# Optimization experiments

Hardware: AMD Instinct MI355X
Metric: run time of the kernel (lower is better)

The kernel has to match this reference:

```python
import jax, jax.numpy as jnp
import numpy as np

B, S, D, H = 4, 2048, 1024, 16
HD = D // H
EPS = 1e-5
MASKED_BIAS = -10000.0

def setup_inputs() -> dict:
    key = jax.random.key(0)
    ks = jax.random.split(key, 12)
    sd = 0.02
    return {
        "hidden_states": jax.random.normal(ks[0], (B, S, D), jnp.float32),
        "Wq": jax.random.normal(ks[1], (D, D), jnp.float32) * sd,
        "bq": jnp.zeros((D,), jnp.float32),
        "Wk": jax.random.normal(ks[2], (D, D), jnp.float32) * sd,
        "bk": jnp.zeros((D,), jnp.float32),
        "Wv": jax.random.normal(ks[3], (D, D), jnp.float32) * sd,
        "bv": jnp.zeros((D,), jnp.float32),
        "Wp": jax.random.normal(ks[4], (D, D), jnp.float32) * sd,
        "bp": jnp.zeros((D,), jnp.float32),
        "ln_g": jnp.ones((D,), jnp.float32),
        "ln_b": jnp.zeros((D,), jnp.float32),
    }

def reference(hidden_states, Wq, bq, Wk, bk, Wv, bv, Wp, bp, ln_g, ln_b):
    x = hidden_states  # [B,S,D]
    # QKV projections (nn.Linear: x @ W^T + b; here W stored as [D,D], use x@W)
    q = x @ Wq + bq
    k = x @ Wk + bk
    v = x @ Wv + bv
    # split heads -> [B,H,S,HD]
    def split(t):
        return t.reshape(B, S, H, HD).transpose(0, 2, 1, 3)
    q, k, v = split(q), split(k), split(v)
    # scaled scores [B,H,S,S]
    scores = jnp.einsum("bhqd,bhkd->bhqk", q, k) / jnp.float32(np.sqrt(HD))
    causal = jnp.tril(jnp.ones((S, S), bool))
    scores = jnp.where(causal[None, None], scores, jnp.float32(MASKED_BIAS))
    attn = jax.nn.softmax(scores, axis=-1)
    out = jnp.einsum("bhqk,bhkd->bhqd", attn, v)
    # merge heads -> [B,S,D]
    out = out.transpose(0, 2, 1, 3).reshape(B, S, D)
    out = out @ Wp + bp
    # residual + layernorm
    y = out + x
    mu = jnp.mean(y, axis=-1, keepdims=True)
    var = jnp.var(y, axis=-1, keepdims=True)
    y = (y - mu) * jax.lax.rsqrt(var + EPS) * ln_g + ln_b
    return y
```

## Files before the change

### kernel.cpp

```cpp
#include <hip/hip_runtime.h>
#include <math.h>

#define B_  4
#define S_  2048
#define D_  1024
#define H_  16
#define HD_ 64
#define M_  (B_*S_)

typedef unsigned int  uint;
typedef unsigned short ushort;

typedef __attribute__((ext_vector_type(8))) short bf16x8;
typedef __attribute__((ext_vector_type(4))) float f32x4;

#if __has_builtin(__builtin_amdgcn_exp2f)
#define EXP2(x) __builtin_amdgcn_exp2f(x)
#else
#define EXP2(x) exp2f(x)
#endif

__device__ __forceinline__ ushort f2bf(float x) {
    uint u = __float_as_uint(x);
    u += 0x7FFFu + ((u >> 16) & 1u);
    return (ushort)(u >> 16);
}
__device__ __forceinline__ uint pack2bf(float a, float b) {
    uint ua = __float_as_uint(a); ua += 0x7FFFu + ((ua >> 16) & 1u);
    uint ub = __float_as_uint(b); ub += 0x7FFFu + ((ub >> 16) & 1u);
    return (ua >> 16) | (ub & 0xFFFF0000u);
}

__global__ __launch_bounds__(256) void prep(const float* __restrict__ x,
                                            ushort* __restrict__ xb,
                                            const float* __restrict__ Wq,
                                            const float* __restrict__ Wk,
                                            const float* __restrict__ Wv,
                                            const float* __restrict__ Wp,
                                            ushort* __restrict__ wtq,
                                            ushort* __restrict__ wtk,
                                            ushort* __restrict__ wtv,
                                            ushort* __restrict__ wtp) {
    __shared__ float t[32][33];
    const int tid = threadIdx.x;
    if (blockIdx.z == 0) {
        const int idx = blockIdx.x * 256 + tid;
        const float4* p = (const float4*)(x + (size_t)idx * 8);
        float4 a = p[0], b = p[1];
        uint4 o;
        o.x = pack2bf(a.x, a.y); o.y = pack2bf(a.z, a.w);
        o.z = pack2bf(b.x, b.y); o.w = pack2bf(b.z, b.w);
        ((uint4*)xb)[idx] = o;
    } else {
        const int w = blockIdx.x >> 10;
        const int sub = blockIdx.x & 1023;
        const float* W = (w == 0) ? Wq : (w == 1) ? Wk : (w == 2) ? Wv : Wp;
        ushort* Wt     = (w == 0) ? wtq : (w == 1) ? wtk : (w == 2) ? wtv : wtp;
        const int nb = (sub & 31) * 32, kb = (sub >> 5) * 32;
        #pragma unroll
        for (int l = 0; l < 4; ++l) {
            int idx = tid + l * 256;
            int r = idx >> 5, c = idx & 31;
            t[r][c] = W[(size_t)(kb + r) * D_ + nb + c];
        }
        __syncthreads();
        #pragma unroll
        for (int l = 0; l < 4; ++l) {
            int idx = tid + l * 256;
            int nr = idx >> 5, kc = idx & 31;
            Wt[(size_t)(nb + nr) * D_ + kb + kc] = f2bf(t[kc][nr]);
        }
    }
}

#define GM 128
#define GN 128
#define GK 64

struct GemmLds {
    ushort As[GM * GK];
    ushort Bs[GN * GK];
};

template <bool SWAP>
__device__ __forceinline__ void gemm_core(GemmLds& L,
                                          const ushort* __restrict__ A,
                                          const ushort* __restrict__ Bt,
                                          f32x4 acc[4][4], int m0, int n0) {
    const int tid  = threadIdx.x;
    const int wave = tid >> 6, lane = tid & 63;
    const int wm = (wave >> 1) * 64, wn = (wave & 1) * 64;
    const int fr = lane & 15, fq = lane >> 4;
    const int xrw = (fr & 7) << 4;

    int sg[4];
    #pragma unroll
    for (int it = 0; it < 4; ++it) {
        const int o = (it * 256 + tid) * 16;
        const int r = o >> 7, c = o & 127;
        sg[it] = r * (D_ * 2) + (c ^ ((r & 7) << 4));
    }

    #pragma unroll
    for (int i = 0; i < 4; ++i)
        #pragma unroll
        for (int j = 0; j < 4; ++j) acc[i][j] = (f32x4){0.f, 0.f, 0.f, 0.f};

    const char* Ab = (const char*)A + (size_t)m0 * (D_ * 2);
    const char* Bb = (const char*)Bt + (size_t)n0 * (D_ * 2);

    for (int k0 = 0; k0 < D_; k0 += GK) {
        #pragma unroll
        for (int it = 0; it < 4; ++it) {
            __builtin_amdgcn_global_load_lds(
                (const __attribute__((address_space(1))) void*)(Ab + k0 * 2 + sg[it]),
                (__attribute__((address_space(3))) void*)(&L.As[(it * 256 + wave * 64) * 8]), 16, 0, 0);
            __builtin_amdgcn_global_load_lds(
                (const __attribute__((address_space(1))) void*)(Bb + k0 * 2 + sg[it]),
                (__attribute__((address_space(3))) void*)(&L.Bs[(it * 256 + wave * 64) * 8]), 16, 0, 0);
        }
        __syncthreads();

        #pragma unroll
        for (int kk = 0; kk < 2; ++kk) {
            bf16x8 af[4], bfr[4];
            #pragma unroll
            for (int i = 0; i < 4; ++i)
                af[i] = *(const bf16x8*)((const char*)L.As + (wm + 16 * i + fr) * 128 + ((kk * 64 + fq * 16) ^ xrw));
            #pragma unroll
            for (int j = 0; j < 4; ++j)
                bfr[j] = *(const bf16x8*)((const char*)L.Bs + (wn + 16 * j + fr) * 128 + ((kk * 64 + fq * 16) ^ xrw));
            #pragma unroll
            for (int i = 0; i < 4; ++i)
                #pragma unroll
                for (int j = 0; j < 4; ++j)
                    acc[i][j] = SWAP
                        ? __builtin_amdgcn_mfma_f32_16x16x32_bf16(bfr[j], af[i], acc[i][j], 0, 0, 0)
                        : __builtin_amdgcn_mfma_f32_16x16x32_bf16(af[i], bfr[j], acc[i][j], 0, 0, 0);
        }
        __syncthreads();
    }
}

__global__ __launch_bounds__(256) void gemm_qkvt(const ushort* __restrict__ xb,
                                                 const ushort* __restrict__ wtq,
                                                 const ushort* __restrict__ wtk,
                                                 const ushort* __restrict__ wtv,
                                                 const float* __restrict__ bq,
                                                 const float* __restrict__ bk,
                                                 const float* __restrict__ bv,
                                                 ushort* __restrict__ qb,
                                                 ushort* __restrict__ kb,
                                                 ushort* __restrict__ vtb) {
    __shared__ __align__(16) GemmLds L;
    const int z = blockIdx.z;
    const int lane = threadIdx.x & 63, wave = threadIdx.x >> 6;
    const int wm = (wave >> 1) * 64, wn = (wave & 1) * 64;
    const int cc = lane & 15, fq = lane >> 4;
    const int m0 = blockIdx.x * GM, n0 = blockIdx.y * GN;
    f32x4 acc[4][4];

    if (z < 2) {
        gemm_core<true>(L, xb, z ? wtk : wtq, acc, m0, n0);
        const float* bias = z ? bk : bq;
        ushort* C = z ? kb : qb;
        const float sc = z ? 1.0f : 0.18033688f;
        #pragma unroll
        for (int j = 0; j < 4; ++j) {
            const int f0 = n0 + wn + 16 * j + fq * 4;
            const float4 bs4 = *(const float4*)&bias[f0];
            const int h = f0 >> 6, hd = f0 & 63;
            #pragma unroll
            for (int i = 0; i < 4; ++i) {
                const int token = m0 + wm + 16 * i + cc;
                const int bb = token >> 11, s = token & 2047;
                const float v0 = (acc[i][j][0] + bs4.x) * sc;
                const float v1 = (acc[i][j][1] + bs4.y) * sc;
                const float v2 = (acc[i][j][2] + bs4.z) * sc;
                const float v3 = (acc[i][j][3] + bs4.w) * sc;
                uint2 w; w.x = pack2bf(v0, v1); w.y = pack2bf(v2, v3);
                *(uint2*)&C[(((size_t)bb * H_ + h) * S_ + s) * HD_ + hd] = w;
            }
        }
    } else {
        gemm_core<false>(L, xb, wtv, acc, m0, n0);
        #pragma unroll
        for (int i = 0; i < 4; ++i) {
            const int t0 = m0 + wm + 16 * i + fq * 4;
            const int bb = t0 >> 11, s = t0 & 2047;
            #pragma unroll
            for (int j = 0; j < 4; ++j) {
                const int f = n0 + wn + 16 * j + cc;
                const float bs = bv[f];
                const int h = f >> 6, hd = f & 63;
                uint2 w;
                w.x = pack2bf(acc[i][j][0] + bs, acc[i][j][1] + bs);
                w.y = pack2bf(acc[i][j][2] + bs, acc[i][j][3] + bs);
                *(uint2*)&vtb[(((size_t)bb * H_ + h) * HD_ + hd) * S_ + s] = w;
            }
        }
    }
}

__global__ __launch_bounds__(256) void gemm_p(const ushort* __restrict__ A,
                                              const ushort* __restrict__ Bt,
                                              const float* __restrict__ bias,
                                              float* __restrict__ C) {
    __shared__ __align__(16) GemmLds L;
    const int m0 = blockIdx.y * GM, n0 = blockIdx.x * GN;
    f32x4 acc[4][4];
    gemm_core<false>(L, A, Bt, acc, m0, n0);

    const int lane = threadIdx.x & 63, wave = threadIdx.x >> 6;
    const int wm = (wave >> 1) * 64, wn = (wave & 1) * 64;
    const int cr = (lane >> 4) * 4, cc = lane & 15;
    #pragma unroll
    for (int j = 0; j < 4; ++j) {
        const int col = n0 + wn + 16 * j + cc;
        const float bs = bias[col];
        #pragma unroll
        for (int i = 0; i < 4; ++i)
            #pragma unroll
            for (int r = 0; r < 4; ++r)
                C[(size_t)(m0 + wm + 16 * i + cr + r) * D_ + col] = acc[i][j][r] + bs;
    }
}

#define PST 72

#define STAGE(kt_, buf_) do {                                                   \
    const int kn_ = (kt_) * 64;                                                 \
    __builtin_amdgcn_global_load_lds(                                           \
        (const __attribute__((address_space(1))) void*)((const char*)kbase + (size_t)kn_ * 128 + kg), \
        (__attribute__((address_space(3))) void*)(&Ks[buf_][wave * 512]), 16, 0, 0); \
    __builtin_amdgcn_global_load_lds(                                           \
        (const __attribute__((address_space(1))) void*)((const char*)vbase + (size_t)kn_ * 2 + vg), \
        (__attribute__((address_space(3))) void*)(&Vs[buf_][wave * 512]), 16, 0, 0); \
} while (0)

__global__ __launch_bounds__(512, 4) void attn_mfma(const ushort* __restrict__ qb,
                                                    const ushort* __restrict__ kb,
                                                    const ushort* __restrict__ vtb,
                                                    ushort* __restrict__ ob) {
    __shared__ __align__(16) ushort Ks[2][64 * 64];
    __shared__ __align__(16) ushort Vs[2][64 * 64];
    __shared__ __align__(16) ushort Pp[8][16 * PST];

    const int tid = threadIdx.x, wave = tid >> 6, lane = tid & 63;
    const int fr = lane & 15, fq = lane >> 4;
    const int hb = blockIdx.x;
    const int p  = blockIdx.y;
    const int b = hb >> 4, h = hb & 15;
    const size_t bh = (size_t)b * H_ + h;
    const ushort* qbase = qb + bh * S_ * HD_;
    const ushort* kbase = kb + bh * S_ * HD_;
    const ushort* vbase = vtb + bh * HD_ * S_;
    ushort* PpW = Pp[wave];
    const int xrw = (fr & 7) << 4;

    int kg, vg;
    {
        const int o = tid * 16;
        const int r = o >> 7, cS = o & 127;
        kg = r * 128 + (cS ^ ((r & 7) << 4));
        vg = r * (S_ * 2) + (cS ^ ((r & 7) << 4));
    }

    for (int phase = 0; phase < 2; ++phase) {
        const int chunk = phase ? p : (15 - p);
        const int q0 = chunk * 128;
        const int wq0 = q0 + wave * 16;
        const int qrow = wq0 + fr;
        const int ntile = 2 * (chunk + 1);

        bf16x8 qf[2];
        #pragma unroll
        for (int kk = 0; kk < 2; ++kk)
            qf[kk] = *(const bf16x8*)&qbase[(size_t)qrow * HD_ + kk * 32 + fq * 8];

        f32x4 ot[4];
        #pragma unroll
        for (int mt = 0; mt < 4; ++mt) ot[mt] = (f32x4){0.f, 0.f, 0.f, 0.f};
        float lp = 0.f;

        int cur = 0;
        STAGE(0, 0);
        __syncthreads();

        for (int t = 0; t < ntile; ++t) {
            if (t + 1 < ntile) STAGE(t + 1, cur ^ 1);
            const ushort* Kb = Ks[cur];
            const ushort* Vb = Vs[cur];
            const int k0 = t * 64;

            f32x4 st[4];
            #pragma unroll
            for (int mt = 0; mt < 4; ++mt) st[mt] = (f32x4){0.f, 0.f, 0.f, 0.f};

            if (t < ntile - 2) {
                #pragma unroll
                for (int kk = 0; kk < 2; ++kk) {
                    bf16x8 kf[4];
                    #pragma unroll
                    for (int mt = 0; mt < 4; ++mt)
                        kf[mt] = *(const bf16x8*)((const char*)Kb + (mt * 16 + fr) * 128 + ((kk * 64 + fq * 16) ^ xrw));
                    __builtin_amdgcn_s_setprio(1);
                    #pragma unroll
                    for (int mt = 0; mt < 4; ++mt)
                        st[mt] = __builtin_amdgcn_mfma_f32_16x16x32_bf16(kf[mt], qf[kk], st[mt], 0, 0, 0);
                    __builtin_amdgcn_s_setprio(0);
                }
                #pragma unroll
                for (int mt = 0; mt < 4; ++mt) {
                    float pr[4];
                    #pragma unroll
                    for (int r = 0; r < 4; ++r) pr[r] = EXP2(st[mt][r]);
                    lp += (pr[0] + pr[1]) + (pr[2] + pr[3]);
                    uint2 w;
                    w.x = pack2bf(pr[0], pr[1]);
                    w.y = pack2bf(pr[2], pr[3]);
                    *(uint2*)&PpW[fr * PST + mt * 16 + fq * 4] = w;
                }
                #pragma unroll
                for (int kk = 0; kk < 2; ++kk) {
                    bf16x8 vf[4];
                    #pragma unroll
                    for (int mt = 0; mt < 4; ++mt)
                        vf[mt] = *(const bf16x8*)((const char*)Vb + (mt * 16 + fr) * 128 + ((kk * 64 + fq * 16) ^ xrw));
                    bf16x8 pf = *(const bf16x8*)&PpW[fr * PST + kk * 32 + fq * 8];
                    __builtin_amdgcn_s_setprio(1);
                    #pragma unroll
                    for (int mt = 0; mt < 4; ++mt)
                        ot[mt] = __builtin_amdgcn_mfma_f32_16x16x32_bf16(vf[mt], pf, ot[mt], 0, 0, 0);
                    __builtin_amdgcn_s_setprio(0);
                }
            } else {
                #pragma unroll
                for (int kk = 0; kk < 2; ++kk) {
                    bf16x8 kf[4];
                    #pragma unroll
                    for (int mt = 0; mt < 4; ++mt)
                        kf[mt] = *(const bf16x8*)((const char*)Kb + (mt * 16 + fr) * 128 + ((kk * 64 + fq * 16) ^ xrw));
                    #pragma unroll
                    for (int mt = 0; mt < 4; ++mt)
                        if (k0 + mt * 16 <= wq0 + 15)
                            st[mt] = __builtin_amdgcn_mfma_f32_16x16x32_bf16(kf[mt], qf[kk], st[mt], 0, 0, 0);
                }
                #pragma unroll
                for (int mt = 0; mt < 4; ++mt) {
                    const int kb0 = k0 + mt * 16 + fq * 4;
                    float pr[4];
                    #pragma unroll
                    for (int r = 0; r < 4; ++r) {
                        const float e = EXP2(st[mt][r]);
                        pr[r] = (kb0 + r > qrow) ? 0.f : e;
                    }
                    lp += (pr[0] + pr[1]) + (pr[2] + pr[3]);
                    uint2 w;
                    w.x = pack2bf(pr[0], pr[1]);
                    w.y = pack2bf(pr[2], pr[3]);
                    *(uint2*)&PpW[fr * PST + mt * 16 + fq * 4] = w;
                }
                #pragma unroll
                for (int kk = 0; kk < 2; ++kk) {
                    if (k0 + kk * 32 <= wq0 + 15) {
                        bf16x8 vf[4];
                        #pragma unroll
                        for (int mt = 0; mt < 4; ++mt)
                            vf[mt] = *(const bf16x8*)((const char*)Vb + (mt * 16 + fr) * 128 + ((kk * 64 + fq * 16) ^ xrw));
                        bf16x8 pf = *(const bf16x8*)&PpW[fr * PST + kk * 32 + fq * 8];
                        #pragma unroll
                        for (int mt = 0; mt < 4; ++mt)
                            ot[mt] = __builtin_amdgcn_mfma_f32_16x16x32_bf16(vf[mt], pf, ot[mt], 0, 0, 0);
                    }
                }
            }
            __syncthreads();
            cur ^= 1;
        }

        float l = lp;
        l += __shfl_xor(l, 16);
        l += __shfl_xor(l, 32);
        const float inv = 1.0f / l;
        #pragma unroll
        for (int mt = 0; mt < 4; ++mt) {
            uint2 w;
            w.x = pack2bf(ot[mt][0] * inv, ot[mt][1] * inv);
            w.y = pack2bf(ot[mt][2] * inv, ot[mt][3] * inv);
            *(uint2*)&ob[((size_t)b * S_ + qrow) * D_ + h * HD_ + mt * 16 + fq * 4] = w;
        }
    }
}

__global__ __launch_bounds__(256) void resln(float* __restrict__ out,
                                             const float* __restrict__ x,
                                             const float* __restrict__ g,
                                             const float* __restrict__ bb) {
    __shared__ float red[256];
    const int row = blockIdx.x, tid = threadIdx.x;
    const size_t off = (size_t)row * D_ + tid * 4;

    float4 p  = *(const float4*)&out[off];
    float4 xr = *(const float4*)&x[off];
    float4 y  = make_float4(p.x + xr.x, p.y + xr.y, p.z + xr.z, p.w + xr.w);

    float sum = y.x + y.y + y.z + y.w;
    red[tid] = sum;
    __syncthreads();
    #pragma unroll
    for (int st = 128; st > 0; st >>= 1) {
        if (tid < st) red[tid] += red[tid + st];
        __syncthreads();
    }
    const float mu = red[0] * (1.0f / D_);
    __syncthreads();

    float dx = y.x - mu, dy = y.y - mu, dz = y.z - mu, dw = y.w - mu;
    red[tid] = dx * dx + dy * dy + dz * dz + dw * dw;
    __syncthreads();
    #pragma unroll
    for (int st = 128; st > 0; st >>= 1) {
        if (tid < st) red[tid] += red[tid + st];
        __syncthreads();
    }
    const float var = red[0] * (1.0f / D_);
    const float inv = rsqrtf(var + 1e-5f);

    float4 gg = *(const float4*)&g[tid * 4];
    float4 bv = *(const float4*)&bb[tid * 4];
    float4 r;
    r.x = dx * inv * gg.x + bv.x;
    r.y = dy * inv * gg.y + bv.y;
    r.z = dz * inv * gg.z + bv.z;
    r.w = dw * inv * gg.w + bv.w;
    *(float4*)&out[off] = r;
}

extern "C" void kernel_launch(void* const* d_in, const int* in_sizes, int n_in,
                              void* d_out, int out_size, void* d_ws, size_t ws_size,
                              hipStream_t stream) {
    const float* x    = (const float*)d_in[0];
    const float* Wq   = (const float*)d_in[1];
    const float* bq   = (const float*)d_in[2];
    const float* Wk   = (const float*)d_in[3];
    const float* bk   = (const float*)d_in[4];
    const float* Wv   = (const float*)d_in[5];
    const float* bv   = (const float*)d_in[6];
    const float* Wp   = (const float*)d_in[7];
    const float* bp   = (const float*)d_in[8];
    const float* ln_g = (const float*)d_in[9];
    const float* ln_b = (const float*)d_in[10];

    float* out = (float*)d_out;

    char* ws = (char*)d_ws;
    ushort* qb  = (ushort*)ws;
    ushort* kb  = (ushort*)(ws + (size_t)16 * (1 << 20));
    ushort* vtb = (ushort*)(ws + (size_t)32 * (1 << 20));
    ushort* xb  = (ushort*)(ws + (size_t)48 * (1 << 20));
    ushort* ob  = (ushort*)(ws + (size_t)64 * (1 << 20));
    ushort* wtq = (ushort*)(ws + (size_t)80 * (1 << 20));
    ushort* wtk = (ushort*)(ws + (size_t)82 * (1 << 20));
    ushort* wtv = (ushort*)(ws + (size_t)84 * (1 << 20));
    ushort* wtp = (ushort*)(ws + (size_t)86 * (1 << 20));

    prep<<<dim3(4096, 1, 2), 256, 0, stream>>>(x, xb, Wq, Wk, Wv, Wp, wtq, wtk, wtv, wtp);

    gemm_qkvt<<<dim3(M_ / GM, D_ / GN, 3), 256, 0, stream>>>(
        xb, wtq, wtk, wtv, bq, bk, bv, qb, kb, vtb);

    attn_mfma<<<dim3(64, 8), 512, 0, stream>>>(qb, kb, vtb, ob);

    gemm_p<<<dim3(D_ / GN, M_ / GM), 256, 0, stream>>>(ob, wtp, bp, out);
    resln<<<M_, 256, 0, stream>>>(out, x, ln_g, ln_b);
}
```

Measured before the change: 280.0 us.

## Double-buffer GEMM LDS tiles with GK 32 to overlap loads and MFMA

```diff
diff --git a/kernel.cpp b/kernel.cpp
--- a/kernel.cpp
+++ b/kernel.cpp
@@ -75,12 +75,23 @@
 
 #define GM 128
 #define GN 128
-#define GK 64
+#define GK 32
 
 struct GemmLds {
-    ushort As[GM * GK];
-    ushort Bs[GN * GK];
+    ushort As[2][GM * GK];
+    ushort Bs[2][GN * GK];
 };
+
+#define GSTAGE(koff_, buf_) do {                                                \
+    _Pragma("unroll")                                                           \
+    for (int it_ = 0; it_ < 2; ++it_) {                                         \
+        __builtin_amdgcn_global_load_lds(                                       \
+            (const __attribute__((address_space(1))) void*)(Ab + (koff_) + sg[it_]), \
+            (__attribute__((address_space(3))) void*)(&L.As[buf_][(it_ * 256 + wave * 64) * 8]), 16, 0, 0); \
+        __builtin_amdgcn_global_load_lds(                                       \
+            (const __attribute__((address_space(1))) void*)(Bb + (koff_) + sg[it_]), \
+            (__attribute__((address_space(3))) void*)(&L.Bs[buf_][(it_ * 256 + wave * 64) * 8]), 16, 0, 0); \
+    } } while (0)
 
 template <bool SWAP>
 __device__ __forceinline__ void gemm_core(GemmLds& L,
@@ -91,14 +102,14 @@
     const int wave = tid >> 6, lane = tid & 63;
     const int wm = (wave >> 1) * 64, wn = (wave & 1) * 64;
     const int fr = lane & 15, fq = lane >> 4;
-    const int xrw = (fr & 7) << 4;
-
-    int sg[4];
+    const int xrw = (fr & 3) << 4;
+
+    int sg[2];
     #pragma unroll
-    for (int it = 0; it < 4; ++it) {
+    for (int it = 0; it < 2; ++it) {
         const int o = (it * 256 + tid) * 16;
-        const int r = o >> 7, c = o & 127;
-        sg[it] = r * (D_ * 2) + (c ^ ((r & 7) << 4));
+        const int r = o >> 6, c = o & 63;
+        sg[it] = r * (D_ * 2) + (c ^ ((r & 3) << 4));
     }
 
     #pragma unroll
@@ -109,36 +120,30 @@
     const char* Ab = (const char*)A + (size_t)m0 * (D_ * 2);
     const char* Bb = (const char*)Bt + (size_t)n0 * (D_ * 2);
 
+    GSTAGE(0, 0);
+    __syncthreads();
+
+    int cur = 0;
     for (int k0 = 0; k0 < D_; k0 += GK) {
-        #pragma unroll
-        for (int it = 0; it < 4; ++it) {
-            __builtin_amdgcn_global_load_lds(
-                (const __attribute__((address_space(1))) void*)(Ab + k0 * 2 + sg[it]),
-                (__attribute__((address_space(3))) void*)(&L.As[(it * 256 + wave * 64) * 8]), 16, 0, 0);
-            __builtin_amdgcn_global_load_lds(
-                (const __attribute__((address_space(1))) void*)(Bb + k0 * 2 + sg[it]),
-                (__attribute__((address_space(3))) void*)(&L.Bs[(it * 256 + wave * 64) * 8]), 16, 0, 0);
-        }
-        __syncthreads();
-
-        #pragma unroll
-        for (int kk = 0; kk < 2; ++kk) {
-            bf16x8 af[4], bfr[4];
-            #pragma unroll
-            for (int i = 0; i < 4; ++i)
-                af[i] = *(const bf16x8*)((const char*)L.As + (wm + 16 * i + fr) * 128 + ((kk * 64 + fq * 16) ^ xrw));
+        if (k0 + GK < D_) GSTAGE((k0 + GK) * 2, cur ^ 1);
+
+        bf16x8 af[4], bfr[4];
+        #pragma unroll
+        for (int i = 0; i < 4; ++i)
+            af[i] = *(const bf16x8*)((const char*)L.As[cur] + (wm + 16 * i + fr) * 64 + ((fq * 16) ^ xrw));
+        #pragma unroll
+        for (int j = 0; j < 4; ++j)
+            bfr[j] = *(const bf16x8*)((const char*)L.Bs[cur] + (wn + 16 * j + fr) * 64 + ((fq * 16) ^ xrw));
+        #pragma unroll
+        for (int i = 0; i < 4; ++i)
             #pragma unroll
             for (int j = 0; j < 4; ++j)
-                bfr[j] = *(const bf16x8*)((const char*)L.Bs + (wn + 16 * j + fr) * 128 + ((kk * 64 + fq * 16) ^ xrw));
-            #pragma unroll
-            for (int i = 0; i < 4; ++i)
-                #pragma unroll
-                for (int j = 0; j < 4; ++j)
-                    acc[i][j] = SWAP
-                        ? __builtin_amdgcn_mfma_f32_16x16x32_bf16(bfr[j], af[i], acc[i][j], 0, 0, 0)
-                        : __builtin_amdgcn_mfma_f32_16x16x32_bf16(af[i], bfr[j], acc[i][j], 0, 0, 0);
-        }
+                acc[i][j] = SWAP
+                    ? __builtin_amdgcn_mfma_f32_16x16x32_bf16(bfr[j], af[i], acc[i][j], 0, 0, 0)
+                    : __builtin_amdgcn_mfma_f32_16x16x32_bf16(af[i], bfr[j], acc[i][j], 0, 0, 0);
+
         __syncthreads();
+        cur ^= 1;
     }
 }
 
```

Result: no change. 285.5 us (+2.0%).
